# Kernel optimization log

Hardware: AMD Instinct MI355X
Metric: run time of the kernel (lower is better)

## Reference

```python
import jax, jax.numpy as jnp
import numpy as np

N_NODES = 500000


def gcn_conv(x, edge_index, W, b, n_nodes):
    # PyG GCNConv: h = x @ W; add self-loops; symmetric deg normalization;
    # scatter-add messages to target nodes; add bias.
    h = x @ W                                # [N, out]
    row, col = edge_index[0], edge_index[1]  # source -> target
    ones = jnp.ones(row.shape, dtype=h.dtype)
    deg = jax.ops.segment_sum(ones, col, num_segments=n_nodes) + 1.0  # +1 self-loop
    dinv = jnp.where(deg > 0, deg ** -0.5, 0.0)
    norm = dinv[row] * dinv[col]             # [E]
    msg = h[row] * norm[:, None]             # [E, out]
    agg = jax.ops.segment_sum(msg, col, num_segments=n_nodes)
    agg = agg + (dinv * dinv)[:, None] * h   # self-loop contribution
    return agg + b


def setup_inputs() -> dict:
    key = jax.random.key(0)
    k1, k2, k3, k4, k5, k6 = jax.random.split(key, 6)
    x = jax.random.normal(k1, (N_NODES, 9), dtype=jnp.float32)
    edge_index = jax.random.randint(k2, (2, 16000000), 0, N_NODES, dtype=jnp.int64)
    # Glorot-style init for GCN weights, zero bias (PyG default bias=True)
    W1 = jax.random.uniform(k3, (9, 4), jnp.float32, -1.0, 1.0) * (6.0 / (9 + 4)) ** 0.5
    b1 = jnp.zeros((4,), jnp.float32)
    W2 = jax.random.uniform(k4, (4, 2), jnp.float32, -1.0, 1.0) * (6.0 / (4 + 2)) ** 0.5
    b2 = jnp.zeros((2,), jnp.float32)
    return {"x": x, "edge_index": edge_index, "W1": W1, "b1": b1, "W2": W2, "b2": b2}


def reference(x, edge_index, W1, b1, W2, b2):
    h = gcn_conv(x, edge_index, W1, b1, N_NODES)
    h = jnp.tanh(h)
    h = gcn_conv(h, edge_index, W2, b2, N_NODES)
    return h
```

## Files before the change

kernel.cpp:

```cpp
#include <hip/hip_runtime.h>
#include <hip/hip_fp16.h>
#include <math.h>

#define NN 500000
#define BSZ 512
#define NBK ((NN + BSZ - 1) / BSZ)
#define SCH 8192
#define KMAX 20
#define SZMAX 17408

typedef __attribute__((ext_vector_type(4))) _Float16 half4;
typedef __attribute__((ext_vector_type(2))) _Float16 half2v;
typedef __attribute__((ext_vector_type(4))) int int4v;
typedef __attribute__((ext_vector_type(2))) float float2v;

__global__ void hist_kernel(const int* __restrict__ col, unsigned short* __restrict__ blkCnt,
                            int E, int nch) {
    __shared__ int cnt[4 * 1024];
    int t = threadIdx.x;
    for (int i = t; i < 4096; i += 256) cnt[i] = 0;
    __syncthreads();
    int base = blockIdx.x * (4 * SCH);
    int end = base + 4 * SCH; if (end > E) end = E;
    for (int j = base + t * 4; j < end; j += 1024) {
        int4v c = __builtin_nontemporal_load(reinterpret_cast<const int4v*>(col + j));
        int sub = (j - base) >> 13;
        atomicAdd(&cnt[sub * 1024 + (c.x >> 9)], 1);
        atomicAdd(&cnt[sub * 1024 + (c.y >> 9)], 1);
        atomicAdd(&cnt[sub * 1024 + (c.z >> 9)], 1);
        atomicAdd(&cnt[sub * 1024 + (c.w >> 9)], 1);
    }
    __syncthreads();
    int chunk0 = blockIdx.x * 4;
#pragma unroll
    for (int s = 0; s < 4; ++s) {
        int c = chunk0 + s;
        if (c >= nch) break;
        for (int b = t; b < 1024; b += 256)
            blkCnt[(size_t)c * 1024 + b] = (unsigned short)cnt[s * 1024 + b];
    }
}

__global__ void colscan_kernel(unsigned short* __restrict__ blkCnt,
                               int* __restrict__ bucketTotal, int nch) {
    __shared__ int ls[64][5];
    int t = threadIdx.x;
    int cl = t & 3;
    int bk = t >> 2;
    int b = blockIdx.x * 4 + cl;
    int cps = (nch + 63) >> 6;
    int c0 = bk * cps;
    int c1 = c0 + cps; if (c1 > nch) c1 = nch;
    int run = 0;
    for (int c = c0; c < c1; ++c)
        run += blkCnt[(size_t)c * 1024 + b];
    ls[bk][cl] = run;
    __syncthreads();
    if (t < 4) {
        int r = 0;
        for (int k = 0; k < 64; ++k) { int v = ls[k][t]; ls[k][t] = r; r += v; }
        bucketTotal[blockIdx.x * 4 + t] = r;
    }
    __syncthreads();
    int running = ls[bk][cl];
    for (int c = c0; c < c1; ++c) {
        size_t idx = (size_t)c * 1024 + b;
        int v = blkCnt[idx];
        blkCnt[idx] = (unsigned short)running;
        running += v;
    }
}

__global__ void scan_kernel(const int* __restrict__ bucketTotal, int* __restrict__ bucketStart) {
    __shared__ int ls[1024];
    int t = threadIdx.x;
    int v = bucketTotal[t];
    ls[t] = v;
    __syncthreads();
    for (int off = 1; off < 1024; off <<= 1) {
        int u = (t >= off) ? ls[t - off] : 0;
        __syncthreads();
        ls[t] += u;
        __syncthreads();
    }
    bucketStart[t] = ls[t] - v;
}

__global__ __launch_bounds__(256) void part_kernel(const int* __restrict__ row,
                                                   const int* __restrict__ col,
                                                   const int* __restrict__ bucketStart,
                                                   const int* __restrict__ bucketTotal,
                                                   const unsigned short* __restrict__ blkPre,
                                                   int* __restrict__ recs, int E, int nch) {
    __shared__ int gbase[1024];
    __shared__ int lexcl[1024];
    __shared__ int cursor[1024];
    __shared__ int ts[256];
    __shared__ int srt[SCH];
    __shared__ unsigned short bkt[SCH];
    int t = threadIdx.x;
    int chunk = blockIdx.x;
    const unsigned short* pre = blkPre + (size_t)chunk * 1024;
    const unsigned short* nxt = blkPre + (size_t)(chunk + 1) * 1024;
    bool last = (chunk == nch - 1);
    int myc[4];
#pragma unroll
    for (int k = 0; k < 4; ++k) {
        int b = t * 4 + k;
        int p = pre[b];
        int n = last ? bucketTotal[b] : (int)nxt[b];
        myc[k] = n - p;
        gbase[b] = bucketStart[b] + p;
    }
    int tsum = myc[0] + myc[1] + myc[2] + myc[3];
    ts[t] = tsum;
    __syncthreads();
    for (int off = 1; off < 256; off <<= 1) {
        int u = (t >= off) ? ts[t - off] : 0;
        __syncthreads();
        ts[t] += u;
        __syncthreads();
    }
    int r = ts[t] - tsum;
#pragma unroll
    for (int k = 0; k < 4; ++k) {
        int b = t * 4 + k;
        lexcl[b] = r;
        cursor[b] = r;
        r += myc[k];
    }
    __syncthreads();
    int base = chunk * SCH;
    int end = base + SCH; if (end > E) end = E;
    for (int j = base + t * 4; j < end; j += 1024) {
        int4v rr = __builtin_nontemporal_load(reinterpret_cast<const int4v*>(row + j));
        int4v cc = __builtin_nontemporal_load(reinterpret_cast<const int4v*>(col + j));
        int b, rk;
        b = cc.x >> 9; rk = atomicAdd(&cursor[b], 1); srt[rk] = (rr.x << 9) | (cc.x & 511); bkt[rk] = (unsigned short)b;
        b = cc.y >> 9; rk = atomicAdd(&cursor[b], 1); srt[rk] = (rr.y << 9) | (cc.y & 511); bkt[rk] = (unsigned short)b;
        b = cc.z >> 9; rk = atomicAdd(&cursor[b], 1); srt[rk] = (rr.z << 9) | (cc.z & 511); bkt[rk] = (unsigned short)b;
        b = cc.w >> 9; rk = atomicAdd(&cursor[b], 1); srt[rk] = (rr.w << 9) | (cc.w & 511); bkt[rk] = (unsigned short)b;
    }
    __syncthreads();
    int m = end - base;
    for (int p = t; p < m; p += 256) {
        int b = bkt[p];
        recs[gbase[b] + (p - lexcl[b])] = srt[p];
    }
}

__global__ __launch_bounds__(1024) void sort_kernel(const int* __restrict__ bucketStart,
                                                    const int* __restrict__ bucketTotal,
                                                    int* __restrict__ recs,
                                                    float* __restrict__ dinv,
                                                    int* __restrict__ nodeStart, int N, int E) {
    __shared__ int cnt[BSZ];
    __shared__ int sc[BSZ];
    __shared__ int srtS[SZMAX];
    int t = threadIdx.x, b = blockIdx.x;
    int s = bucketStart[b], m = bucketTotal[b];
    int v[KMAX];
#pragma unroll
    for (int k = 0; k < KMAX; ++k) {
        int idx = t + k * 1024;
        v[k] = (idx < m) ? recs[s + idx] : -1;
    }
    if (t < BSZ) cnt[t] = 0;
    __syncthreads();
#pragma unroll
    for (int k = 0; k < KMAX; ++k)
        if (v[k] >= 0) atomicAdd(&cnt[v[k] & 511], 1);
    __syncthreads();
    if (t < BSZ) sc[t] = cnt[t];
    __syncthreads();
    for (int off = 1; off < BSZ; off <<= 1) {
        int u = 0;
        if (t < BSZ && t >= off) u = sc[t - off];
        __syncthreads();
        if (t < BSZ) sc[t] += u;
        __syncthreads();
    }
    if (t < BSZ) {
        int excl = sc[t] - cnt[t];
        int node = b * BSZ + t;
        if (node < N) {
            nodeStart[node] = s + excl;
            dinv[node] = rsqrtf((float)cnt[t] + 1.0f);
        }
        cnt[t] = excl;
    }
    if (b == NBK - 1 && t == 0) nodeStart[N] = E;
    __syncthreads();
#pragma unroll
    for (int k = 0; k < KMAX; ++k) {
        if (v[k] >= 0) {
            int rk = atomicAdd(&cnt[v[k] & 511], 1);
            srtS[rk] = v[k] >> 9;
        }
    }
    __syncthreads();
    for (int p = t; p < m; p += 1024)
        recs[s + p] = srtS[p];
}

__global__ __launch_bounds__(256) void prep_kernel(const float* __restrict__ x,
                                                   const float* __restrict__ W1,
                                                   const float* __restrict__ dinv,
                                                   half4* __restrict__ g1h, int N) {
    __shared__ float xs[256 * 9];
    int t = threadIdx.x;
    int base = blockIdx.x * 256;
    int nval = (N - base < 256 ? N - base : 256) * 9;
    const float* xb = x + (size_t)base * 9;
    for (int k = t; k < nval; k += 256) xs[k] = xb[k];
    __syncthreads();
    int i = base + t;
    if (i >= N) return;
    float d = dinv[i];
    float acc0 = 0.f, acc1 = 0.f, acc2 = 0.f, acc3 = 0.f;
#pragma unroll
    for (int k = 0; k < 9; ++k) {
        float xv = xs[t * 9 + k];
        acc0 += xv * W1[k * 4 + 0];
        acc1 += xv * W1[k * 4 + 1];
        acc2 += xv * W1[k * 4 + 2];
        acc3 += xv * W1[k * 4 + 3];
    }
    half4 h;
    h.x = (_Float16)(d * acc0);
    h.y = (_Float16)(d * acc1);
    h.z = (_Float16)(d * acc2);
    h.w = (_Float16)(d * acc3);
    g1h[i] = h;
}

#define NTL(p) __builtin_nontemporal_load(p)

__global__ __launch_bounds__(256) void agg1_kernel(const int* __restrict__ nodeStart,
                                                   const int* __restrict__ srows,
                                                   const float* __restrict__ dinv,
                                                   const half4* __restrict__ g1h,
                                                   const float* __restrict__ b1,
                                                   const float* __restrict__ W2,
                                                   half2v* __restrict__ g2h, int N) {
    int i = blockIdx.x * blockDim.x + threadIdx.x;
    if (i >= N) return;
    int s = nodeStart[i], e = nodeStart[i + 1];
    float a0 = 0.f, a1 = 0.f, a2 = 0.f, a3 = 0.f;
    int j = s;
    for (; j < e && (j & 3); ++j) {
        half4 g = g1h[NTL(srows + j)];
        a0 += (float)g.x; a1 += (float)g.y; a2 += (float)g.z; a3 += (float)g.w;
    }
    for (; j + 15 < e; j += 16) {
        int4v q0 = NTL(reinterpret_cast<const int4v*>(srows + j));
        int4v q1 = NTL(reinterpret_cast<const int4v*>(srows + j + 4));
        int4v q2 = NTL(reinterpret_cast<const int4v*>(srows + j + 8));
        int4v q3 = NTL(reinterpret_cast<const int4v*>(srows + j + 12));
        half4 g0 = g1h[q0.x], g1 = g1h[q0.y], g2 = g1h[q0.z], g3 = g1h[q0.w];
        half4 g4 = g1h[q1.x], g5 = g1h[q1.y], g6 = g1h[q1.z], g7 = g1h[q1.w];
        half4 g8 = g1h[q2.x], g9 = g1h[q2.y], gA = g1h[q2.z], gB = g1h[q2.w];
        half4 gC = g1h[q3.x], gD = g1h[q3.y], gE = g1h[q3.z], gF = g1h[q3.w];
        a0 += (((float)g0.x + (float)g1.x) + ((float)g2.x + (float)g3.x)) +
              (((float)g4.x + (float)g5.x) + ((float)g6.x + (float)g7.x)) +
              (((float)g8.x + (float)g9.x) + ((float)gA.x + (float)gB.x)) +
              (((float)gC.x + (float)gD.x) + ((float)gE.x + (float)gF.x));
        a1 += (((float)g0.y + (float)g1.y) + ((float)g2.y + (float)g3.y)) +
              (((float)g4.y + (float)g5.y) + ((float)g6.y + (float)g7.y)) +
              (((float)g8.y + (float)g9.y) + ((float)gA.y + (float)gB.y)) +
              (((float)gC.y + (float)gD.y) + ((float)gE.y + (float)gF.y));
        a2 += (((float)g0.z + (float)g1.z) + ((float)g2.z + (float)g3.z)) +
              (((float)g4.z + (float)g5.z) + ((float)g6.z + (float)g7.z)) +
              (((float)g8.z + (float)g9.z) + ((float)gA.z + (float)gB.z)) +
              (((float)gC.z + (float)gD.z) + ((float)gE.z + (float)gF.z));
        a3 += (((float)g0.w + (float)g1.w) + ((float)g2.w + (float)g3.w)) +
              (((float)g4.w + (float)g5.w) + ((float)g6.w + (float)g7.w)) +
              (((float)g8.w + (float)g9.w) + ((float)gA.w + (float)gB.w)) +
              (((float)gC.w + (float)gD.w) + ((float)gE.w + (float)gF.w));
    }
    for (; j + 3 < e; j += 4) {
        int4v r4 = NTL(reinterpret_cast<const int4v*>(srows + j));
        half4 g0 = g1h[r4.x];
        half4 g1 = g1h[r4.y];
        half4 g2 = g1h[r4.z];
        half4 g3 = g1h[r4.w];
        a0 += ((float)g0.x + (float)g1.x) + ((float)g2.x + (float)g3.x);
        a1 += ((float)g0.y + (float)g1.y) + ((float)g2.y + (float)g3.y);
        a2 += ((float)g0.z + (float)g1.z) + ((float)g2.z + (float)g3.z);
        a3 += ((float)g0.w + (float)g1.w) + ((float)g2.w + (float)g3.w);
    }
    for (; j < e; ++j) {
        half4 g = g1h[NTL(srows + j)];
        a0 += (float)g.x; a1 += (float)g.y; a2 += (float)g.z; a3 += (float)g.w;
    }
    half4 self = g1h[i];
    float di = dinv[i];
    float t0 = tanhf(di * (a0 + (float)self.x) + b1[0]);
    float t1 = tanhf(di * (a1 + (float)self.y) + b1[1]);
    float t2 = tanhf(di * (a2 + (float)self.z) + b1[2]);
    float t3 = tanhf(di * (a3 + (float)self.w) + b1[3]);
    float o0 = t0 * W2[0] + t1 * W2[2] + t2 * W2[4] + t3 * W2[6];
    float o1 = t0 * W2[1] + t1 * W2[3] + t2 * W2[5] + t3 * W2[7];
    half2v g2o;
    g2o.x = (_Float16)(di * o0);
    g2o.y = (_Float16)(di * o1);
    g2h[i] = g2o;
}

__global__ __launch_bounds__(256) void agg2_kernel(const int* __restrict__ nodeStart,
                                                   const int* __restrict__ srows,
                                                   const float* __restrict__ dinv,
                                                   const half2v* __restrict__ g2h,
                                                   const float* __restrict__ b2,
                                                   float* __restrict__ out, int N) {
    int i = blockIdx.x * blockDim.x + threadIdx.x;
    if (i >= N) return;
    int s = nodeStart[i], e = nodeStart[i + 1];
    float a0 = 0.f, a1 = 0.f;
    int j = s;
    for (; j < e && (j & 3); ++j) {
        half2v g = g2h[NTL(srows + j)];
        a0 += (float)g.x; a1 += (float)g.y;
    }
    for (; j + 15 < e; j += 16) {
        int4v q0 = NTL(reinterpret_cast<const int4v*>(srows + j));
        int4v q1 = NTL(reinterpret_cast<const int4v*>(srows + j + 4));
        int4v q2 = NTL(reinterpret_cast<const int4v*>(srows + j + 8));
        int4v q3 = NTL(reinterpret_cast<const int4v*>(srows + j + 12));
        half2v g0 = g2h[q0.x], g1 = g2h[q0.y], g2 = g2h[q0.z], g3 = g2h[q0.w];
        half2v g4 = g2h[q1.x], g5 = g2h[q1.y], g6 = g2h[q1.z], g7 = g2h[q1.w];
        half2v g8 = g2h[q2.x], g9 = g2h[q2.y], gA = g2h[q2.z], gB = g2h[q2.w];
        half2v gC = g2h[q3.x], gD = g2h[q3.y], gE = g2h[q3.z], gF = g2h[q3.w];
        a0 += (((float)g0.x + (float)g1.x) + ((float)g2.x + (float)g3.x)) +
              (((float)g4.x + (float)g5.x) + ((float)g6.x + (float)g7.x)) +
              (((float)g8.x + (float)g9.x) + ((float)gA.x + (float)gB.x)) +
              (((float)gC.x + (float)gD.x) + ((float)gE.x + (float)gF.x));
        a1 += (((float)g0.y + (float)g1.y) + ((float)g2.y + (float)g3.y)) +
              (((float)g4.y + (float)g5.y) + ((float)g6.y + (float)g7.y)) +
              (((float)g8.y + (float)g9.y) + ((float)gA.y + (float)gB.y)) +
              (((float)gC.y + (float)gD.y) + ((float)gE.y + (float)gF.y));
    }
    for (; j + 3 < e; j += 4) {
        int4v r4 = NTL(reinterpret_cast<const int4v*>(srows + j));
        half2v g0 = g2h[r4.x];
        half2v g1 = g2h[r4.y];
        half2v g2 = g2h[r4.z];
        half2v g3 = g2h[r4.w];
        a0 += ((float)g0.x + (float)g1.x) + ((float)g2.x + (float)g3.x);
        a1 += ((float)g0.y + (float)g1.y) + ((float)g2.y + (float)g3.y);
    }
    for (; j < e; ++j) {
        half2v g = g2h[NTL(srows + j)];
        a0 += (float)g.x; a1 += (float)g.y;
    }
    half2v self = g2h[i];
    float di = dinv[i];
    float2v o;
    o.x = di * (a0 + (float)self.x) + b2[0];
    o.y = di * (a1 + (float)self.y) + b2[1];
    __builtin_nontemporal_store(o, reinterpret_cast<float2v*>(out) + i);
}

extern "C" void kernel_launch(void* const* d_in, const int* in_sizes, int n_in,
                              void* d_out, int out_size, void* d_ws, size_t ws_size,
                              hipStream_t stream) {
    const float* x  = (const float*)d_in[0];
    const int*   ei = (const int*)d_in[1];
    const float* W1 = (const float*)d_in[2];
    const float* b1 = (const float*)d_in[3];
    const float* W2 = (const float*)d_in[4];
    const float* b2 = (const float*)d_in[5];
    float* out = (float*)d_out;

    const int N = NN;
    const int E = in_sizes[1] / 2;
    const int* row = ei;
    const int* col = ei + E;

    const int nch = (E + SCH - 1) / SCH;

    char* ws = (char*)d_ws;
    size_t off = 0;
    int* bucketTotal = (int*)(ws + off);            off += 4096;
    int* bucketStart = (int*)(ws + off);            off += 4096;
    off = 16384;
    unsigned short* blkCnt = (unsigned short*)(ws + off);
    off += (size_t)(nch + 1) * 1024 * 2;
    off = (off + 15) & ~(size_t)15;
    float*  dinv      = (float*)(ws + off);         off += (size_t)NN * 4;
    off = (off + 15) & ~(size_t)15;
    half4*  g1h       = (half4*)(ws + off);         off += (size_t)NN * 8;
    off = (off + 15) & ~(size_t)15;
    half2v* g2h       = (half2v*)(ws + off);        off += (size_t)NN * 4;
    off = (off + 15) & ~(size_t)15;
    int*    nodeStart = (int*)(ws + off);           off += (size_t)(NN + 1) * 4;
    off = (off + 15) & ~(size_t)15;
    int*    recs      = (int*)(ws + off);

    (void)hipMemsetAsync(blkCnt + (size_t)nch * 1024, 0, 2048, stream);

    const int ngrid = (N + 255) / 256;
    const int hgrid = (nch + 3) / 4;

    hist_kernel   <<<hgrid, 256, 0, stream>>>(col, blkCnt, E, nch);
    colscan_kernel<<<256, 256, 0, stream>>>(blkCnt, bucketTotal, nch);
    scan_kernel   <<<1, 1024, 0, stream>>>(bucketTotal, bucketStart);
    part_kernel   <<<nch, 256, 0, stream>>>(row, col, bucketStart, bucketTotal, blkCnt, recs, E, nch);
    sort_kernel   <<<NBK, 1024, 0, stream>>>(bucketStart, bucketTotal, recs, dinv, nodeStart, N, E);
    prep_kernel   <<<ngrid, 256, 0, stream>>>(x, W1, dinv, g1h, N);
    agg1_kernel   <<<ngrid, 256, 0, stream>>>(nodeStart, recs, dinv, g1h, b1, W2, g2h, N);
    agg2_kernel   <<<ngrid, 256, 0, stream>>>(nodeStart, recs, dinv, g2h, b2, out, N);
}
```

Measured before the change: 592.4 us.

## Sort nodes by degree within each bucket to balance warp work in aggregation

The sort kernel now builds a per-bucket counting sort of nodes by in-degree (capped at 128) and writes a node permutation. Both aggregation kernels map threads to nodes through this permutation, so lanes in a wavefront handle nodes of similar degree and less time is lost to divergence. The cost is an extra indirection load, a serial 129-entry scan in the sort kernel, and scattered writes to the node-indexed outputs and nodeStart/dinv reads.

```diff
diff --git a/kernel.cpp b/kernel.cpp
--- a/kernel.cpp
+++ b/kernel.cpp
@@ -153,9 +153,11 @@
                                                     const int* __restrict__ bucketTotal,
                                                     int* __restrict__ recs,
                                                     float* __restrict__ dinv,
-                                                    int* __restrict__ nodeStart, int N, int E) {
+                                                    int* __restrict__ nodeStart,
+                                                    int* __restrict__ nodePerm, int N, int E) {
     __shared__ int cnt[BSZ];
     __shared__ int sc[BSZ];
+    __shared__ int dh[129];
     __shared__ int srtS[SZMAX];
     int t = threadIdx.x, b = blockIdx.x;
     int s = bucketStart[b], m = bucketTotal[b];
@@ -180,16 +182,33 @@
         if (t < BSZ) sc[t] += u;
         __syncthreads();
     }
+    int node = b * BSZ + t;
+    bool valid = (t < BSZ) && (node < N);
+    int myDeg = 0;
     if (t < BSZ) {
-        int excl = sc[t] - cnt[t];
-        int node = b * BSZ + t;
+        myDeg = cnt[t];
+        int excl = sc[t] - myDeg;
         if (node < N) {
             nodeStart[node] = s + excl;
-            dinv[node] = rsqrtf((float)cnt[t] + 1.0f);
+            dinv[node] = rsqrtf((float)myDeg + 1.0f);
         }
         cnt[t] = excl;
     }
     if (b == NBK - 1 && t == 0) nodeStart[N] = E;
+    if (t < 129) dh[t] = 0;
+    __syncthreads();
+    int dmin = myDeg > 128 ? 128 : myDeg;
+    if (valid) atomicAdd(&dh[dmin], 1);
+    __syncthreads();
+    if (t == 0) {
+        int r = 0;
+        for (int k = 0; k < 129; ++k) { int u = dh[k]; dh[k] = r; r += u; }
+    }
+    __syncthreads();
+    if (valid) {
+        int rk = atomicAdd(&dh[dmin], 1);
+        nodePerm[b * BSZ + rk] = node;
+    }
     __syncthreads();
 #pragma unroll
     for (int k = 0; k < KMAX; ++k) {
@@ -242,9 +261,11 @@
                                                    const half4* __restrict__ g1h,
                                                    const float* __restrict__ b1,
                                                    const float* __restrict__ W2,
+                                                   const int* __restrict__ nodePerm,
                                                    half2v* __restrict__ g2h, int N) {
-    int i = blockIdx.x * blockDim.x + threadIdx.x;
-    if (i >= N) return;
+    int gid = blockIdx.x * blockDim.x + threadIdx.x;
+    if (gid >= N) return;
+    int i = nodePerm[gid];
     int s = nodeStart[i], e = nodeStart[i + 1];
     float a0 = 0.f, a1 = 0.f, a2 = 0.f, a3 = 0.f;
     int j = s;
@@ -312,9 +333,11 @@
                                                    const float* __restrict__ dinv,
                                                    const half2v* __restrict__ g2h,
                                                    const float* __restrict__ b2,
+                                                   const int* __restrict__ nodePerm,
                                                    float* __restrict__ out, int N) {
-    int i = blockIdx.x * blockDim.x + threadIdx.x;
-    if (i >= N) return;
+    int gid = blockIdx.x * blockDim.x + threadIdx.x;
+    if (gid >= N) return;
+    int i = nodePerm[gid];
     int s = nodeStart[i], e = nodeStart[i + 1];
     float a0 = 0.f, a1 = 0.f;
     int j = s;
@@ -395,6 +418,8 @@
     off = (off + 15) & ~(size_t)15;
     int*    nodeStart = (int*)(ws + off);           off += (size_t)(NN + 1) * 4;
     off = (off + 15) & ~(size_t)15;
+    int*    nodePerm  = (int*)(ws + off);           off += (size_t)NN * 4;
+    off = (off + 15) & ~(size_t)15;
     int*    recs      = (int*)(ws + off);
 
     (void)hipMemsetAsync(blkCnt + (size_t)nch * 1024, 0, 2048, stream);
@@ -406,8 +431,8 @@
     colscan_kernel<<<256, 256, 0, stream>>>(blkCnt, bucketTotal, nch);
     scan_kernel   <<<1, 1024, 0, stream>>>(bucketTotal, bucketStart);
     part_kernel   <<<nch, 256, 0, stream>>>(row, col, bucketStart, bucketTotal, blkCnt, recs, E, nch);
-    sort_kernel   <<<NBK, 1024, 0, stream>>>(bucketStart, bucketTotal, recs, dinv, nodeStart, N, E);
+    sort_kernel   <<<NBK, 1024, 0, stream>>>(bucketStart, bucketTotal, recs, dinv, nodeStart, nodePerm, N, E);
     prep_kernel   <<<ngrid, 256, 0, stream>>>(x, W1, dinv, g1h, N);
-    agg1_kernel   <<<ngrid, 256, 0, stream>>>(nodeStart, recs, dinv, g1h, b1, W2, g2h, N);
-    agg2_kernel   <<<ngrid, 256, 0, stream>>>(nodeStart, recs, dinv, g2h, b2, out, N);
-}
+    agg1_kernel   <<<ngrid, 256, 0, stream>>>(nodeStart, recs, dinv, g1h, b1, W2, nodePerm, g2h, N);
+    agg2_kernel   <<<ngrid, 256, 0, stream>>>(nodeStart, recs, dinv, g2h, b2, nodePerm, out, N);
+}
```

New measurement: 626.7 us. 5.8% more time.
